# Kernel tuning notes

Hardware: AMD Instinct MI355X
Metric: run time of the kernel (lower is better)

## Reference

```python
import jax, jax.numpy as jnp
import numpy as np


def _squash_dim2(s):
    # Original: n = s.norm(2, dim=2, keepdim=True); dim 2 is singleton for s,
    # so n == |s| elementwise. scale = n^2/(1+n^2); out = scale * s / n.
    n2 = jnp.sum(s * s, axis=2, keepdims=True)
    n = jnp.sqrt(n2)
    return (n2 / (1.0 + n2)) * s / n


def setup_inputs() -> dict:
    key = jax.random.key(0)
    k1, k2 = jax.random.split(key)
    B, N, Cin = 256, 1152, 8
    K, Cout = 10, 16
    x = jax.random.normal(k1, (B, N, Cin), dtype=jnp.float32)
    routing_weights = jax.random.normal(k2, (K, N, Cin, Cout), dtype=jnp.float32)
    return {"x": x, "routing_weights": routing_weights, "num_iterations": 3}


def reference(x, routing_weights, num_iterations):
    # prediction_vectors: x[None,:,:,None,:] @ W[:,None] -> [K, B, N, 1, Cout]
    pred = jnp.einsum('bni,knio->kbno', x, routing_weights)[:, :, :, None, :]
    logits = jnp.zeros_like(pred)  # [K, B, N, 1, Cout]
    v = None
    for _ in range(num_iterations):
        # batch_softmax: cat over dim0 -> [K*B, N, 1, Cout]; legacy F.softmax
        # on 4D uses dim=1 => softmax over route-nodes axis (axis=2 here).
        c = jax.nn.softmax(logits, axis=2)
        s = jnp.sum(c * pred, axis=2, keepdims=True)  # [K, B, 1, 1, Cout]
        v = _squash_dim2(s)
        logits = logits + pred * v
    return v  # [K, B, 1, 1, Cout]
```

## Files before the change

### kernel.cpp

```cpp
#include <hip/hip_runtime.h>
#include <hip/hip_bf16.h>

#define BDIM 256
#define NDIM 1152
#define CIN 8
#define KDIM 10
#define COUT 16
#define NTHREADS 512
#define BT 2
#define NPT 9


#if defined(__has_builtin)
#  if __has_builtin(__builtin_amdgcn_exp2f)
#    define EXP2F(x) __builtin_amdgcn_exp2f(x)
#  endif
#endif
#ifndef EXP2F
#  define EXP2F(x) exp2f(x)
#endif
#define LOG2E 1.4426950408889634f

__device__ __forceinline__ unsigned pack2(float a, float b) {
    union { __hip_bfloat162 h; unsigned u; } cv;
    cv.h = __float22bfloat162_rn(make_float2(a, b));
    return cv.u;
}
__device__ __forceinline__ float bf_lo(unsigned u) { return __uint_as_float(u << 16); }
__device__ __forceinline__ float bf_hi(unsigned u) { return __uint_as_float(u & 0xffff0000u); }

__global__ __attribute__((amdgpu_flat_work_group_size(NTHREADS, NTHREADS),
                          amdgpu_waves_per_eu(4, 4)))
void capsule_routing_kernel(const float* __restrict__ x,
                            const float* __restrict__ w,
                            const int*   __restrict__ niter_p,
                            float*       __restrict__ out)
{
    __shared__ uint4  predS[NDIM * 4];
    __shared__ float4 redP[8][4][2];
    __shared__ float4 redI[2][8][4][4];

    const int blk = blockIdx.x;
    const int k   = blk >> 7;
    const int b0  = (blk & 127) * BT;
    const int t   = threadIdx.x;
    const int wv  = t >> 6;
    const int l   = t & 63;
    const int coq = t & 3;
    const int nb  = t >> 2;

    const float* __restrict__ xb0 = x + (size_t)b0 * NDIM * CIN;
    const float* __restrict__ xb1 = xb0 + NDIM * CIN;
    const float* __restrict__ wk  = w + (size_t)k * NDIM * CIN * COUT + coq * 4;

    float ps0[4] = {0.f,0.f,0.f,0.f}, ps1[4] = {0.f,0.f,0.f,0.f};

#pragma unroll 1
    for (int j = 0; j < NPT; ++j) {
        const int n = nb + 128 * j;
        const float4 xa0 = *reinterpret_cast<const float4*>(xb0 + n * CIN);
        const float4 xc0 = *reinterpret_cast<const float4*>(xb0 + n * CIN + 4);
        const float4 xa1 = *reinterpret_cast<const float4*>(xb1 + n * CIN);
        const float4 xc1 = *reinterpret_cast<const float4*>(xb1 + n * CIN + 4);
        const float xs0[8] = {xa0.x,xa0.y,xa0.z,xa0.w,xc0.x,xc0.y,xc0.z,xc0.w};
        const float xs1[8] = {xa1.x,xa1.y,xa1.z,xa1.w,xc1.x,xc1.y,xc1.z,xc1.w};
        const float* wr = wk + (size_t)n * (CIN * COUT);
        float a0[4] = {0.f,0.f,0.f,0.f}, a1[4] = {0.f,0.f,0.f,0.f};
#pragma unroll
        for (int i = 0; i < CIN; ++i) {
            const float4 w4 = *reinterpret_cast<const float4*>(wr + i * COUT);
            a0[0] = fmaf(xs0[i], w4.x, a0[0]);
            a0[1] = fmaf(xs0[i], w4.y, a0[1]);
            a0[2] = fmaf(xs0[i], w4.z, a0[2]);
            a0[3] = fmaf(xs0[i], w4.w, a0[3]);
            a1[0] = fmaf(xs1[i], w4.x, a1[0]);
            a1[1] = fmaf(xs1[i], w4.y, a1[1]);
            a1[2] = fmaf(xs1[i], w4.z, a1[2]);
            a1[3] = fmaf(xs1[i], w4.w, a1[3]);
        }
        uint4 qq;
        qq.x = pack2(a0[0], a0[1]);
        qq.y = pack2(a0[2], a0[3]);
        qq.z = pack2(a1[0], a1[1]);
        qq.w = pack2(a1[2], a1[3]);
        predS[n * 4 + coq] = qq;
#pragma unroll
        for (int c = 0; c < 4; ++c) { ps0[c] += a0[c]; ps1[c] += a1[c]; }
    }

#pragma unroll
    for (int m = 4; m < 64; m <<= 1) {
#pragma unroll
        for (int c = 0; c < 4; ++c) {
            ps0[c] += __shfl_xor(ps0[c], m, 64);
            ps1[c] += __shfl_xor(ps1[c], m, 64);
        }
    }
    if (l < 4) {
        redP[wv][l][0] = make_float4(ps0[0], ps0[1], ps0[2], ps0[3]);
        redP[wv][l][1] = make_float4(ps1[0], ps1[1], ps1[2], ps1[3]);
    }
    __syncthreads();
    float sT0[4] = {0.f,0.f,0.f,0.f}, sT1[4] = {0.f,0.f,0.f,0.f};
#pragma unroll
    for (int wvi = 0; wvi < 8; ++wvi) {
        const float4 r0 = redP[wvi][coq][0];
        const float4 r1 = redP[wvi][coq][1];
        sT0[0] += r0.x; sT0[1] += r0.y; sT0[2] += r0.z; sT0[3] += r0.w;
        sT1[0] += r1.x; sT1[1] += r1.y; sT1[2] += r1.z; sT1[3] += r1.w;
    }

    const int niter = *niter_p;

    float v0[4], v1[4], vc0[4], vc1[4];
    {
        const float inv = 1.0f / (float)NDIM;
#pragma unroll
        for (int c = 0; c < 4; ++c) {
            const float s0 = sT0[c] * inv;
            const float s1 = sT1[c] * inv;
            v0[c] = s0 * fabsf(s0) / (1.f + s0 * s0);
            v1[c] = s1 * fabsf(s1) / (1.f + s1 * s1);
            vc0[c] = v0[c];
            vc1[c] = v1[c];
        }
    }

    for (int it = 1; it < niter; ++it) {
        const int itb = it & 1;
        float vl0[4], vl1[4];
#pragma unroll
        for (int c = 0; c < 4; ++c) { vl0[c] = vc0[c] * LOG2E; vl1[c] = vc1[c] * LOG2E; }

        float se0[4]={0.f,0.f,0.f,0.f}, sp0[4]={0.f,0.f,0.f,0.f};
        float se1[4]={0.f,0.f,0.f,0.f}, sp1[4]={0.f,0.f,0.f,0.f};
#pragma unroll 3
        for (int j = 0; j < NPT; ++j) {
            const int n = nb + 128 * j;
            const uint4 q = predS[n * 4 + coq];
            const float p0[4] = {bf_lo(q.x), bf_hi(q.x), bf_lo(q.y), bf_hi(q.y)};
            const float p1[4] = {bf_lo(q.z), bf_hi(q.z), bf_lo(q.w), bf_hi(q.w)};
#pragma unroll
            for (int c = 0; c < 4; ++c) {
                const float e0 = EXP2F(p0[c] * vl0[c]);
                se0[c] += e0;
                sp0[c] = fmaf(e0, p0[c], sp0[c]);
                const float e1 = EXP2F(p1[c] * vl1[c]);
                se1[c] += e1;
                sp1[c] = fmaf(e1, p1[c], sp1[c]);
            }
        }
#pragma unroll
        for (int m = 4; m < 64; m <<= 1) {
#pragma unroll
            for (int c = 0; c < 4; ++c) {
                se0[c] += __shfl_xor(se0[c], m, 64);
                sp0[c] += __shfl_xor(sp0[c], m, 64);
                se1[c] += __shfl_xor(se1[c], m, 64);
                sp1[c] += __shfl_xor(sp1[c], m, 64);
            }
        }
        if (l < 4) {
            redI[itb][wv][l][0] = make_float4(se0[0], se0[1], se0[2], se0[3]);
            redI[itb][wv][l][1] = make_float4(sp0[0], sp0[1], sp0[2], sp0[3]);
            redI[itb][wv][l][2] = make_float4(se1[0], se1[1], se1[2], se1[3]);
            redI[itb][wv][l][3] = make_float4(sp1[0], sp1[1], sp1[2], sp1[3]);
        }
        __syncthreads();
        float seT0[4]={0.f,0.f,0.f,0.f}, spT0[4]={0.f,0.f,0.f,0.f};
        float seT1[4]={0.f,0.f,0.f,0.f}, spT1[4]={0.f,0.f,0.f,0.f};
#pragma unroll
        for (int wvi = 0; wvi < 8; ++wvi) {
            const float4 a = redI[itb][wvi][coq][0];
            const float4 b = redI[itb][wvi][coq][1];
            const float4 c4 = redI[itb][wvi][coq][2];
            const float4 d = redI[itb][wvi][coq][3];
            seT0[0]+=a.x; seT0[1]+=a.y; seT0[2]+=a.z; seT0[3]+=a.w;
            spT0[0]+=b.x; spT0[1]+=b.y; spT0[2]+=b.z; spT0[3]+=b.w;
            seT1[0]+=c4.x; seT1[1]+=c4.y; seT1[2]+=c4.z; seT1[3]+=c4.w;
            spT1[0]+=d.x; spT1[1]+=d.y; spT1[2]+=d.z; spT1[3]+=d.w;
        }
#pragma unroll
        for (int c = 0; c < 4; ++c) {
            const float s0 = spT0[c] / seT0[c];
            const float s1 = spT1[c] / seT1[c];
            v0[c] = s0 * fabsf(s0) / (1.f + s0 * s0);
            v1[c] = s1 * fabsf(s1) / (1.f + s1 * s1);
            vc0[c] += v0[c];
            vc1[c] += v1[c];
        }
    }

    if (t < 4) {
        float4 o0, o1;
        o0.x = v0[0]; o0.y = v0[1]; o0.z = v0[2]; o0.w = v0[3];
        o1.x = v1[0]; o1.y = v1[1]; o1.z = v1[2]; o1.w = v1[3];
        *reinterpret_cast<float4*>(out + ((size_t)k * BDIM + b0)     * COUT + t * 4) = o0;
        *reinterpret_cast<float4*>(out + ((size_t)k * BDIM + b0 + 1) * COUT + t * 4) = o1;
    }
}

extern "C" void kernel_launch(void* const* d_in, const int* in_sizes, int n_in,
                              void* d_out, int out_size, void* d_ws, size_t ws_size,
                              hipStream_t stream) {
    const float* x = (const float*)d_in[0];
    const float* w = (const float*)d_in[1];
    const int* niter = (const int*)d_in[2];
    float* out = (float*)d_out;

    const int grid = KDIM * (BDIM / BT);
    capsule_routing_kernel<<<grid, NTHREADS, 0, stream>>>(x, w, niter, out);
}
```

Baseline: 65.84 us.

## Process four batch rows per block to reuse weight loads, use rcp squash

Each block now handles four batch rows instead of two, so each weight float4 loaded from global memory feeds twice as many FMAs and the grid halves to 640 blocks. Shared memory for the bf16 predictions doubles, and waves-per-EU drops to 2 to give the extra accumulators register room. The squash step is rewritten algebraically, folding the 1/N and sp/se divisions into a single hardware reciprocal, and sched_barriers split the weight-load/FMA phases. The risks are lower occupancy, fewer blocks for latency hiding, and a small precision change from using approximate rcp.

```diff
diff --git a/kernel.cpp b/kernel.cpp
--- a/kernel.cpp
+++ b/kernel.cpp
@@ -7,7 +7,7 @@
 #define KDIM 10
 #define COUT 16
 #define NTHREADS 512
-#define BT 2
+#define BT 4
 #define NPT 9
 
 
@@ -15,9 +15,15 @@
 #  if __has_builtin(__builtin_amdgcn_exp2f)
 #    define EXP2F(x) __builtin_amdgcn_exp2f(x)
 #  endif
+#  if __has_builtin(__builtin_amdgcn_rcpf)
+#    define RCPF(x) __builtin_amdgcn_rcpf(x)
+#  endif
 #endif
 #ifndef EXP2F
 #  define EXP2F(x) exp2f(x)
+#endif
+#ifndef RCPF
+#  define RCPF(x) (1.0f / (x))
 #endif
 #define LOG2E 1.4426950408889634f
 
@@ -29,20 +35,38 @@
 __device__ __forceinline__ float bf_lo(unsigned u) { return __uint_as_float(u << 16); }
 __device__ __forceinline__ float bf_hi(unsigned u) { return __uint_as_float(u & 0xffff0000u); }
 
+#define FMA16(i, w4)                                                     \
+    a0[0] = fmaf(xs0[i], (w4).x, a0[0]);                                 \
+    a0[1] = fmaf(xs0[i], (w4).y, a0[1]);                                 \
+    a0[2] = fmaf(xs0[i], (w4).z, a0[2]);                                 \
+    a0[3] = fmaf(xs0[i], (w4).w, a0[3]);                                 \
+    a1[0] = fmaf(xs1[i], (w4).x, a1[0]);                                 \
+    a1[1] = fmaf(xs1[i], (w4).y, a1[1]);                                 \
+    a1[2] = fmaf(xs1[i], (w4).z, a1[2]);                                 \
+    a1[3] = fmaf(xs1[i], (w4).w, a1[3]);                                 \
+    a2[0] = fmaf(xs2[i], (w4).x, a2[0]);                                 \
+    a2[1] = fmaf(xs2[i], (w4).y, a2[1]);                                 \
+    a2[2] = fmaf(xs2[i], (w4).z, a2[2]);                                 \
+    a2[3] = fmaf(xs2[i], (w4).w, a2[3]);                                 \
+    a3[0] = fmaf(xs3[i], (w4).x, a3[0]);                                 \
+    a3[1] = fmaf(xs3[i], (w4).y, a3[1]);                                 \
+    a3[2] = fmaf(xs3[i], (w4).z, a3[2]);                                 \
+    a3[3] = fmaf(xs3[i], (w4).w, a3[3]);
+
 __global__ __attribute__((amdgpu_flat_work_group_size(NTHREADS, NTHREADS),
-                          amdgpu_waves_per_eu(4, 4)))
+                          amdgpu_waves_per_eu(2, 2)))
 void capsule_routing_kernel(const float* __restrict__ x,
                             const float* __restrict__ w,
                             const int*   __restrict__ niter_p,
                             float*       __restrict__ out)
 {
-    __shared__ uint4  predS[NDIM * 4];
-    __shared__ float4 redP[8][4][2];
-    __shared__ float4 redI[2][8][4][4];
+    __shared__ uint4  predS[2][NDIM * 4];
+    __shared__ float4 redP[8][4][BT];
+    __shared__ float4 redI[2][8][4][2*BT];
 
     const int blk = blockIdx.x;
-    const int k   = blk >> 7;
-    const int b0  = (blk & 127) * BT;
+    const int k   = blk >> 6;
+    const int b0  = (blk & 63) * BT;
     const int t   = threadIdx.x;
     const int wv  = t >> 6;
     const int l   = t & 63;
@@ -51,9 +75,12 @@
 
     const float* __restrict__ xb0 = x + (size_t)b0 * NDIM * CIN;
     const float* __restrict__ xb1 = xb0 + NDIM * CIN;
+    const float* __restrict__ xb2 = xb1 + NDIM * CIN;
+    const float* __restrict__ xb3 = xb2 + NDIM * CIN;
     const float* __restrict__ wk  = w + (size_t)k * NDIM * CIN * COUT + coq * 4;
 
     float ps0[4] = {0.f,0.f,0.f,0.f}, ps1[4] = {0.f,0.f,0.f,0.f};
+    float ps2[4] = {0.f,0.f,0.f,0.f}, ps3[4] = {0.f,0.f,0.f,0.f};
 
 #pragma unroll 1
     for (int j = 0; j < NPT; ++j) {
@@ -62,30 +89,56 @@
         const float4 xc0 = *reinterpret_cast<const float4*>(xb0 + n * CIN + 4);
         const float4 xa1 = *reinterpret_cast<const float4*>(xb1 + n * CIN);
         const float4 xc1 = *reinterpret_cast<const float4*>(xb1 + n * CIN + 4);
+        const float4 xa2 = *reinterpret_cast<const float4*>(xb2 + n * CIN);
+        const float4 xc2 = *reinterpret_cast<const float4*>(xb2 + n * CIN + 4);
+        const float4 xa3 = *reinterpret_cast<const float4*>(xb3 + n * CIN);
+        const float4 xc3 = *reinterpret_cast<const float4*>(xb3 + n * CIN + 4);
         const float xs0[8] = {xa0.x,xa0.y,xa0.z,xa0.w,xc0.x,xc0.y,xc0.z,xc0.w};
         const float xs1[8] = {xa1.x,xa1.y,xa1.z,xa1.w,xc1.x,xc1.y,xc1.z,xc1.w};
+        const float xs2[8] = {xa2.x,xa2.y,xa2.z,xa2.w,xc2.x,xc2.y,xc2.z,xc2.w};
+        const float xs3[8] = {xa3.x,xa3.y,xa3.z,xa3.w,xc3.x,xc3.y,xc3.z,xc3.w};
         const float* wr = wk + (size_t)n * (CIN * COUT);
         float a0[4] = {0.f,0.f,0.f,0.f}, a1[4] = {0.f,0.f,0.f,0.f};
-#pragma unroll
-        for (int i = 0; i < CIN; ++i) {
-            const float4 w4 = *reinterpret_cast<const float4*>(wr + i * COUT);
-            a0[0] = fmaf(xs0[i], w4.x, a0[0]);
-            a0[1] = fmaf(xs0[i], w4.y, a0[1]);
-            a0[2] = fmaf(xs0[i], w4.z, a0[2]);
-            a0[3] = fmaf(xs0[i], w4.w, a0[3]);
-            a1[0] = fmaf(xs1[i], w4.x, a1[0]);
-            a1[1] = fmaf(xs1[i], w4.y, a1[1]);
-            a1[2] = fmaf(xs1[i], w4.z, a1[2]);
-            a1[3] = fmaf(xs1[i], w4.w, a1[3]);
-        }
-        uint4 qq;
-        qq.x = pack2(a0[0], a0[1]);
-        qq.y = pack2(a0[2], a0[3]);
-        qq.z = pack2(a1[0], a1[1]);
-        qq.w = pack2(a1[2], a1[3]);
-        predS[n * 4 + coq] = qq;
-#pragma unroll
-        for (int c = 0; c < 4; ++c) { ps0[c] += a0[c]; ps1[c] += a1[c]; }
+        float a2[4] = {0.f,0.f,0.f,0.f}, a3[4] = {0.f,0.f,0.f,0.f};
+        {
+            const float4 wA = *reinterpret_cast<const float4*>(wr);
+            const float4 wB = *reinterpret_cast<const float4*>(wr + COUT);
+            FMA16(0, wA); FMA16(1, wB);
+        }
+        __builtin_amdgcn_sched_barrier(0);
+        {
+            const float4 wA = *reinterpret_cast<const float4*>(wr + 2 * COUT);
+            const float4 wB = *reinterpret_cast<const float4*>(wr + 3 * COUT);
+            FMA16(2, wA); FMA16(3, wB);
+        }
+        __builtin_amdgcn_sched_barrier(0);
+        {
+            const float4 wA = *reinterpret_cast<const float4*>(wr + 4 * COUT);
+            const float4 wB = *reinterpret_cast<const float4*>(wr + 5 * COUT);
+            FMA16(4, wA); FMA16(5, wB);
+        }
+        __builtin_amdgcn_sched_barrier(0);
+        {
+            const float4 wA = *reinterpret_cast<const float4*>(wr + 6 * COUT);
+            const float4 wB = *reinterpret_cast<const float4*>(wr + 7 * COUT);
+            FMA16(6, wA); FMA16(7, wB);
+        }
+        uint4 qA, qB;
+        qA.x = pack2(a0[0], a0[1]);
+        qA.y = pack2(a0[2], a0[3]);
+        qA.z = pack2(a1[0], a1[1]);
+        qA.w = pack2(a1[2], a1[3]);
+        qB.x = pack2(a2[0], a2[1]);
+        qB.y = pack2(a2[2], a2[3]);
+        qB.z = pack2(a3[0], a3[1]);
+        qB.w = pack2(a3[2], a3[3]);
+        predS[0][n * 4 + coq] = qA;
+        predS[1][n * 4 + coq] = qB;
+#pragma unroll
+        for (int c = 0; c < 4; ++c) {
+            ps0[c] += a0[c]; ps1[c] += a1[c];
+            ps2[c] += a2[c]; ps3[c] += a3[c];
+        }
     }
 
 #pragma unroll
@@ -94,60 +147,78 @@
         for (int c = 0; c < 4; ++c) {
             ps0[c] += __shfl_xor(ps0[c], m, 64);
             ps1[c] += __shfl_xor(ps1[c], m, 64);
+            ps2[c] += __shfl_xor(ps2[c], m, 64);
+            ps3[c] += __shfl_xor(ps3[c], m, 64);
         }
     }
     if (l < 4) {
         redP[wv][l][0] = make_float4(ps0[0], ps0[1], ps0[2], ps0[3]);
         redP[wv][l][1] = make_float4(ps1[0], ps1[1], ps1[2], ps1[3]);
+        redP[wv][l][2] = make_float4(ps2[0], ps2[1], ps2[2], ps2[3]);
+        redP[wv][l][3] = make_float4(ps3[0], ps3[1], ps3[2], ps3[3]);
     }
     __syncthreads();
     float sT0[4] = {0.f,0.f,0.f,0.f}, sT1[4] = {0.f,0.f,0.f,0.f};
-#pragma unroll
+    float sT2[4] = {0.f,0.f,0.f,0.f}, sT3[4] = {0.f,0.f,0.f,0.f};
+#pragma unroll 1
     for (int wvi = 0; wvi < 8; ++wvi) {
         const float4 r0 = redP[wvi][coq][0];
         const float4 r1 = redP[wvi][coq][1];
+        const float4 r2 = redP[wvi][coq][2];
+        const float4 r3 = redP[wvi][coq][3];
         sT0[0] += r0.x; sT0[1] += r0.y; sT0[2] += r0.z; sT0[3] += r0.w;
         sT1[0] += r1.x; sT1[1] += r1.y; sT1[2] += r1.z; sT1[3] += r1.w;
+        sT2[0] += r2.x; sT2[1] += r2.y; sT2[2] += r2.z; sT2[3] += r2.w;
+        sT3[0] += r3.x; sT3[1] += r3.y; sT3[2] += r3.z; sT3[3] += r3.w;
     }
 
     const int niter = *niter_p;
 
-    float v0[4], v1[4], vc0[4], vc1[4];
+    float v0[4], v1[4], v2[4], v3[4];
+    float vc0[4], vc1[4], vc2[4], vc3[4];
     {
-        const float inv = 1.0f / (float)NDIM;
-#pragma unroll
-        for (int c = 0; c < 4; ++c) {
-            const float s0 = sT0[c] * inv;
-            const float s1 = sT1[c] * inv;
-            v0[c] = s0 * fabsf(s0) / (1.f + s0 * s0);
-            v1[c] = s1 * fabsf(s1) / (1.f + s1 * s1);
-            vc0[c] = v0[c];
-            vc1[c] = v1[c];
+        const float N2 = (float)NDIM * (float)NDIM;
+#pragma unroll
+        for (int c = 0; c < 4; ++c) {
+            v0[c] = sT0[c] * fabsf(sT0[c]) * RCPF(fmaf(sT0[c], sT0[c], N2));
+            v1[c] = sT1[c] * fabsf(sT1[c]) * RCPF(fmaf(sT1[c], sT1[c], N2));
+            v2[c] = sT2[c] * fabsf(sT2[c]) * RCPF(fmaf(sT2[c], sT2[c], N2));
+            v3[c] = sT3[c] * fabsf(sT3[c]) * RCPF(fmaf(sT3[c], sT3[c], N2));
+            vc0[c] = v0[c]; vc1[c] = v1[c]; vc2[c] = v2[c]; vc3[c] = v3[c];
         }
     }
 
     for (int it = 1; it < niter; ++it) {
         const int itb = it & 1;
-        float vl0[4], vl1[4];
-#pragma unroll
-        for (int c = 0; c < 4; ++c) { vl0[c] = vc0[c] * LOG2E; vl1[c] = vc1[c] * LOG2E; }
-
+        float vl0[4], vl1[4], vl2[4], vl3[4];
+#pragma unroll
+        for (int c = 0; c < 4; ++c) {
+            vl0[c] = vc0[c] * LOG2E; vl1[c] = vc1[c] * LOG2E;
+            vl2[c] = vc2[c] * LOG2E; vl3[c] = vc3[c] * LOG2E;
+        }
         float se0[4]={0.f,0.f,0.f,0.f}, sp0[4]={0.f,0.f,0.f,0.f};
         float se1[4]={0.f,0.f,0.f,0.f}, sp1[4]={0.f,0.f,0.f,0.f};
-#pragma unroll 3
+        float se2[4]={0.f,0.f,0.f,0.f}, sp2[4]={0.f,0.f,0.f,0.f};
+        float se3[4]={0.f,0.f,0.f,0.f}, sp3[4]={0.f,0.f,0.f,0.f};
+#pragma unroll 1
         for (int j = 0; j < NPT; ++j) {
             const int n = nb + 128 * j;
-            const uint4 q = predS[n * 4 + coq];
-            const float p0[4] = {bf_lo(q.x), bf_hi(q.x), bf_lo(q.y), bf_hi(q.y)};
-            const float p1[4] = {bf_lo(q.z), bf_hi(q.z), bf_lo(q.w), bf_hi(q.w)};
+            const uint4 qA = predS[0][n * 4 + coq];
+            const uint4 qB = predS[1][n * 4 + coq];
+            const float p0[4] = {bf_lo(qA.x), bf_hi(qA.x), bf_lo(qA.y), bf_hi(qA.y)};
+            const float p1[4] = {bf_lo(qA.z), bf_hi(qA.z), bf_lo(qA.w), bf_hi(qA.w)};
+            const float p2[4] = {bf_lo(qB.x), bf_hi(qB.x), bf_lo(qB.y), bf_hi(qB.y)};
+            const float p3[4] = {bf_lo(qB.z), bf_hi(qB.z), bf_lo(qB.w), bf_hi(qB.w)};
 #pragma unroll
             for (int c = 0; c < 4; ++c) {
                 const float e0 = EXP2F(p0[c] * vl0[c]);
-                se0[c] += e0;
-                sp0[c] = fmaf(e0, p0[c], sp0[c]);
+                se0[c] += e0; sp0[c] = fmaf(e0, p0[c], sp0[c]);
                 const float e1 = EXP2F(p1[c] * vl1[c]);
-                se1[c] += e1;
-                sp1[c] = fmaf(e1, p1[c], sp1[c]);
+                se1[c] += e1; sp1[c] = fmaf(e1, p1[c], sp1[c]);
+                const float e2 = EXP2F(p2[c] * vl2[c]);
+                se2[c] += e2; sp2[c] = fmaf(e2, p2[c], sp2[c]);
+                const float e3 = EXP2F(p3[c] * vl3[c]);
+                se3[c] += e3; sp3[c] = fmaf(e3, p3[c], sp3[c]);
             }
         }
 #pragma unroll
@@ -158,45 +229,71 @@
                 sp0[c] += __shfl_xor(sp0[c], m, 64);
                 se1[c] += __shfl_xor(se1[c], m, 64);
                 sp1[c] += __shfl_xor(sp1[c], m, 64);
+                se2[c] += __shfl_xor(se2[c], m, 64);
+                sp2[c] += __shfl_xor(sp2[c], m, 64);
+                se3[c] += __shfl_xor(se3[c], m, 64);
+                sp3[c] += __shfl_xor(sp3[c], m, 64);
             }
         }
         if (l < 4) {
             redI[itb][wv][l][0] = make_float4(se0[0], se0[1], se0[2], se0[3]);
-            redI[itb][wv][l][1] = make_float4(sp0[0], sp0[1], sp0[2], sp0[3]);
-            redI[itb][wv][l][2] = make_float4(se1[0], se1[1], se1[2], se1[3]);
-            redI[itb][wv][l][3] = make_float4(sp1[0], sp1[1], sp1[2], sp1[3]);
+            redI[itb][wv][l][1] = make_float4(se1[0], se1[1], se1[2], se1[3]);
+            redI[itb][wv][l][2] = make_float4(se2[0], se2[1], se2[2], se2[3]);
+            redI[itb][wv][l][3] = make_float4(se3[0], se3[1], se3[2], se3[3]);
+            redI[itb][wv][l][4] = make_float4(sp0[0], sp0[1], sp0[2], sp0[3]);
+            redI[itb][wv][l][5] = make_float4(sp1[0], sp1[1], sp1[2], sp1[3]);
+            redI[itb][wv][l][6] = make_float4(sp2[0], sp2[1], sp2[2], sp2[3]);
+            redI[itb][wv][l][7] = make_float4(sp3[0], sp3[1], sp3[2], sp3[3]);
         }
         __syncthreads();
         float seT0[4]={0.f,0.f,0.f,0.f}, spT0[4]={0.f,0.f,0.f,0.f};
         float seT1[4]={0.f,0.f,0.f,0.f}, spT1[4]={0.f,0.f,0.f,0.f};
-#pragma unroll
+        float seT2[4]={0.f,0.f,0.f,0.f}, spT2[4]={0.f,0.f,0.f,0.f};
+        float seT3[4]={0.f,0.f,0.f,0.f}, spT3[4]={0.f,0.f,0.f,0.f};
+#pragma unroll 1
         for (int wvi = 0; wvi < 8; ++wvi) {
-            const float4 a = redI[itb][wvi][coq][0];
-            const float4 b = redI[itb][wvi][coq][1];
-            const float4 c4 = redI[itb][wvi][coq][2];
-            const float4 d = redI[itb][wvi][coq][3];
-            seT0[0]+=a.x; seT0[1]+=a.y; seT0[2]+=a.z; seT0[3]+=a.w;
-            spT0[0]+=b.x; spT0[1]+=b.y; spT0[2]+=b.z; spT0[3]+=b.w;
-            seT1[0]+=c4.x; seT1[1]+=c4.y; seT1[2]+=c4.z; seT1[3]+=c4.w;
-            spT1[0]+=d.x; spT1[1]+=d.y; spT1[2]+=d.z; spT1[3]+=d.w;
-        }
-#pragma unroll
-        for (int c = 0; c < 4; ++c) {
-            const float s0 = spT0[c] / seT0[c];
-            const float s1 = spT1[c] / seT1[c];
-            v0[c] = s0 * fabsf(s0) / (1.f + s0 * s0);
-            v1[c] = s1 * fabsf(s1) / (1.f + s1 * s1);
-            vc0[c] += v0[c];
-            vc1[c] += v1[c];
+            const float4 ra = redI[itb][wvi][coq][0];
+            const float4 rb = redI[itb][wvi][coq][1];
+            const float4 rc = redI[itb][wvi][coq][2];
+            const float4 rd = redI[itb][wvi][coq][3];
+            seT0[0]+=ra.x; seT0[1]+=ra.y; seT0[2]+=ra.z; seT0[3]+=ra.w;
+            seT1[0]+=rb.x; seT1[1]+=rb.y; seT1[2]+=rb.z; seT1[3]+=rb.w;
+            seT2[0]+=rc.x; seT2[1]+=rc.y; seT2[2]+=rc.z; seT2[3]+=rc.w;
+            seT3[0]+=rd.x; seT3[1]+=rd.y; seT3[2]+=rd.z; seT3[3]+=rd.w;
+            const float4 re = redI[itb][wvi][coq][4];
+            const float4 rf = redI[itb][wvi][coq][5];
+            const float4 rg = redI[itb][wvi][coq][6];
+            const float4 rh = redI[itb][wvi][coq][7];
+            spT0[0]+=re.x; spT0[1]+=re.y; spT0[2]+=re.z; spT0[3]+=re.w;
+            spT1[0]+=rf.x; spT1[1]+=rf.y; spT1[2]+=rf.z; spT1[3]+=rf.w;
+            spT2[0]+=rg.x; spT2[1]+=rg.y; spT2[2]+=rg.z; spT2[3]+=rg.w;
+            spT3[0]+=rh.x; spT3[1]+=rh.y; spT3[2]+=rh.z; spT3[3]+=rh.w;
+        }
+#pragma unroll
+        for (int c = 0; c < 4; ++c) {
+            v0[c] = spT0[c] * fabsf(spT0[c]) *
+                    RCPF(fmaf(seT0[c], seT0[c], spT0[c] * spT0[c]));
+            v1[c] = spT1[c] * fabsf(spT1[c]) *
+                    RCPF(fmaf(seT1[c], seT1[c], spT1[c] * spT1[c]));
+            v2[c] = spT2[c] * fabsf(spT2[c]) *
+                    RCPF(fmaf(seT2[c], seT2[c], spT2[c] * spT2[c]));
+            v3[c] = spT3[c] * fabsf(spT3[c]) *
+                    RCPF(fmaf(seT3[c], seT3[c], spT3[c] * spT3[c]));
+            vc0[c] += v0[c]; vc1[c] += v1[c];
+            vc2[c] += v2[c]; vc3[c] += v3[c];
         }
     }
 
     if (t < 4) {
-        float4 o0, o1;
-        o0.x = v0[0]; o0.y = v0[1]; o0.z = v0[2]; o0.w = v0[3];
-        o1.x = v1[0]; o1.y = v1[1]; o1.z = v1[2]; o1.w = v1[3];
-        *reinterpret_cast<float4*>(out + ((size_t)k * BDIM + b0)     * COUT + t * 4) = o0;
-        *reinterpret_cast<float4*>(out + ((size_t)k * BDIM + b0 + 1) * COUT + t * 4) = o1;
+        float4 o;
+        o = make_float4(v0[0], v0[1], v0[2], v0[3]);
+        *reinterpret_cast<float4*>(out + ((size_t)k * BDIM + b0)     * COUT + t * 4) = o;
+        o = make_float4(v1[0], v1[1], v1[2], v1[3]);
+        *reinterpret_cast<float4*>(out + ((size_t)k * BDIM + b0 + 1) * COUT + t * 4) = o;
+        o = make_float4(v2[0], v2[1], v2[2], v2[3]);
+        *reinterpret_cast<float4*>(out + ((size_t)k * BDIM + b0 + 2) * COUT + t * 4) = o;
+        o = make_float4(v3[0], v3[1], v3[2], v3[3]);
+        *reinterpret_cast<float4*>(out + ((size_t)k * BDIM + b0 + 3) * COUT + t * 4) = o;
     }
 }
 
```

Result: slower. 82.05 us (+24.6%).
